# Kernel optimization log

Hardware: AMD Instinct MI355X
Metric: run time of the kernel (lower is better)

Reference implementation:

```python
import jax, jax.numpy as jnp
import numpy as np


def setup_inputs() -> dict:
    key = jax.random.key(0)
    B, N = 4, 32768
    xyz = jax.random.normal(key, (B, N, 3), dtype=jnp.float32)
    return {"xyz": xyz, "K": 16, "nqueries": 2048}


def reference(xyz, K, nqueries):
    # xyz: (b, n, 3). Deterministic strided pick of nqueries query points
    # (stand-in for the KD-tree's distance-pick sampling), then brute-force KNN.
    b, n, _ = xyz.shape
    stride = n // nqueries
    q_idx = jnp.arange(nqueries) * stride          # (nq,)
    pts = xyz[:, q_idx, :]                          # (b, nq, 3) sampled query points
    # pairwise squared distances (b, nq, n)
    d = jnp.sum((pts[:, :, None, :] - xyz[:, None, :, :]) ** 2, axis=-1)
    _, idx = jax.lax.top_k(-d, K)                   # (b, nq, K) nearest-neighbor indices
    idx = idx.astype(jnp.int64)[..., None]          # (b, nq, K, 1) matches expand_dims(..., 3)
    return idx, pts
```

## Files before the change

### kernel.cpp

```cpp
#include <hip/hip_runtime.h>
#include <stdint.h>

#define NPTS  32768
#define NQ    2048
#define KNN   16
#define NB    4
#define BLOCK 256
#define WPB   4
#define PPL   8
#define ITERS (NPTS / (64 * PPL))
#define GATE_MARGIN 5e-4f

__device__ __forceinline__ int dpp_shr1_i(int x) {
    return __builtin_amdgcn_update_dpp(x, x, 0x111, 0xf, 0xf, false);
}
__device__ __forceinline__ float dpp_shr1_f(float x) {
    return __int_as_float(dpp_shr1_i(__float_as_int(x)));
}
__device__ __forceinline__ float readlane_f(float x, int l) {
    return __int_as_float(__builtin_amdgcn_readlane(__float_as_int(x), l));
}

template <int T>
__device__ __forceinline__ void insert_all(float d, int p, int lane,
                                           float& ld, int& li, float& tau,
                                           float& th, float qnm)
{
    unsigned long long rem = __ballot(d <= tau);
    while (rem) {
        const int srcl = __ffsll(rem) - 1;
        const float wd = readlane_f(d, srcl);
        const int   wi = __builtin_amdgcn_readlane(p, srcl);
        const bool less = (ld < wd) || (ld == wd && li < wi);
        const unsigned long long lm = __ballot(less);
        const int pos = __popc((unsigned)((lm >> (16 * T)) & 0xffffull));
        const float pld = dpp_shr1_f(ld);
        const int   pli = dpp_shr1_i(li);
        if ((lane >> 4) == T) {
            const int gl = lane & 15;
            if (gl == pos)      { ld = wd;  li = wi;  }
            else if (gl > pos)  { ld = pld; li = pli; }
        }
        tau = readlane_f(ld, 16 * T + 15);
        th  = tau + qnm;
        rem &= rem - 1;
        if (rem) rem &= __ballot(d <= tau);
    }
}

__device__ __forceinline__ void load6(float4 dst[6], const float4* p) {
    #pragma unroll
    for (int t = 0; t < 6; ++t) dst[t] = p[t];
}

__device__ __forceinline__ void step2(const float4 c[6], int pb, int lane,
                                      float m2x0, float m2y0, float m2z0,
                                      float m2x1, float m2y1, float m2z1,
                                      float qx0, float qy0, float qz0,
                                      float qx1, float qy1, float qz1,
                                      float& ld, int& li,
                                      float& tau0, float& tau1,
                                      float& th0, float& th1,
                                      float qnm0, float qnm1)
{
    float px[PPL], py[PPL], pz[PPL];
    px[0] = c[0].x; py[0] = c[0].y; pz[0] = c[0].z;
    px[1] = c[0].w; py[1] = c[1].x; pz[1] = c[1].y;
    px[2] = c[1].z; py[2] = c[1].w; pz[2] = c[2].x;
    px[3] = c[2].y; py[3] = c[2].z; pz[3] = c[2].w;
    px[4] = c[3].x; py[4] = c[3].y; pz[4] = c[3].z;
    px[5] = c[3].w; py[5] = c[4].x; pz[5] = c[4].y;
    px[6] = c[4].z; py[6] = c[4].w; pz[6] = c[5].x;
    px[7] = c[5].y; py[7] = c[5].z; pz[7] = c[5].w;

    unsigned long long m0[PPL], m1[PPL], any = 0;
    #pragma unroll
    for (int j = 0; j < PPL; ++j) {
        const float s = __fmaf_rn(pz[j], pz[j],
                          __fmaf_rn(py[j], py[j], __fmul_rn(px[j], px[j])));
        float t0 = __fmaf_rn(px[j], m2x0, s);
        t0 = __fmaf_rn(py[j], m2y0, t0);
        t0 = __fmaf_rn(pz[j], m2z0, t0);
        m0[j] = __ballot(t0 <= th0);
        float t1 = __fmaf_rn(px[j], m2x1, s);
        t1 = __fmaf_rn(py[j], m2y1, t1);
        t1 = __fmaf_rn(pz[j], m2z1, t1);
        m1[j] = __ballot(t1 <= th1);
        any |= m0[j] | m1[j];
    }
    if (any) {
        #pragma unroll
        for (int j = 0; j < PPL; ++j) {
            if (m0[j]) {
                const float dx = __fadd_rn(px[j], -qx0);
                const float dy = __fadd_rn(py[j], -qy0);
                const float dz = __fadd_rn(pz[j], -qz0);
                const float d  = __fadd_rn(
                    __fadd_rn(__fmul_rn(dx, dx), __fmul_rn(dy, dy)),
                    __fmul_rn(dz, dz));
                insert_all<0>(d, pb + j, lane, ld, li, tau0, th0, qnm0);
            }
        }
        #pragma unroll
        for (int j = 0; j < PPL; ++j) {
            if (m1[j]) {
                const float dx = __fadd_rn(px[j], -qx1);
                const float dy = __fadd_rn(py[j], -qy1);
                const float dz = __fadd_rn(pz[j], -qz1);
                const float d  = __fadd_rn(
                    __fadd_rn(__fmul_rn(dx, dx), __fmul_rn(dy, dy)),
                    __fmul_rn(dz, dz));
                insert_all<1>(d, pb + j, lane, ld, li, tau1, th1, qnm1);
            }
        }
    }
}

__global__ __launch_bounds__(BLOCK, 4) void knn_kernel(const float* __restrict__ xyz,
                                                       float* __restrict__ out_idx,
                                                       float* __restrict__ out_pts)
{
    const int tid  = threadIdx.x;
    const int lane = tid & 63;
    const int wv   = tid >> 6;
    const int w    = blockIdx.x * WPB + wv;
    const int b    = w >> 10;
    const int pr   = w & 1023;
    const size_t base = (size_t)b * NPTS * 3;

    const int qp0 = pr << 5;
    const float qx0 = xyz[base + 3 * qp0 + 0];
    const float qy0 = xyz[base + 3 * qp0 + 1];
    const float qz0 = xyz[base + 3 * qp0 + 2];
    const float qx1 = xyz[base + 3 * qp0 + 48];
    const float qy1 = xyz[base + 3 * qp0 + 49];
    const float qz1 = xyz[base + 3 * qp0 + 50];

    const int g0 = b * NQ + (pr << 1);
    if (lane == 0) {
        out_pts[3 * g0 + 0] = qx0;
        out_pts[3 * g0 + 1] = qy0;
        out_pts[3 * g0 + 2] = qz0;
        out_pts[3 * g0 + 3] = qx1;
        out_pts[3 * g0 + 4] = qy1;
        out_pts[3 * g0 + 5] = qz1;
    }

    const float m2x0 = -2.0f * qx0, m2y0 = -2.0f * qy0, m2z0 = -2.0f * qz0;
    const float m2x1 = -2.0f * qx1, m2y1 = -2.0f * qy1, m2z1 = -2.0f * qz1;
    const float qnm0 = -(qx0 * qx0 + qy0 * qy0 + qz0 * qz0) + GATE_MARGIN;
    const float qnm1 = -(qx1 * qx1 + qy1 * qy1 + qz1 * qz1) + GATE_MARGIN;

    float ld = __builtin_inff();  int li = 0x7fffffff;
    float tau0 = __builtin_inff(), tau1 = __builtin_inff();
    float th0  = __builtin_inff(), th1  = __builtin_inff();

    const float4* lp0 = (const float4*)(xyz + base) + 6 * lane;

    float4 A[6], Bf[6], Cf[6];
    load6(A,  lp0);
    load6(Bf, lp0 + 384);
    load6(Cf, lp0 + 768);
    const float4* ld_ptr = lp0 + 3 * 384;
    int pb = PPL * lane;

    for (int it = 0; it < 21; ++it) {
        step2(A, pb, lane,
              m2x0, m2y0, m2z0, m2x1, m2y1, m2z1,
              qx0, qy0, qz0, qx1, qy1, qz1,
              ld, li, tau0, tau1, th0, th1, qnm0, qnm1);
        pb += 512;
        load6(A, ld_ptr);  ld_ptr += 384;
        step2(Bf, pb, lane,
              m2x0, m2y0, m2z0, m2x1, m2y1, m2z1,
              qx0, qy0, qz0, qx1, qy1, qz1,
              ld, li, tau0, tau1, th0, th1, qnm0, qnm1);
        pb += 512;
        if (it < 20) load6(Bf, ld_ptr);
        ld_ptr += 384;
        step2(Cf, pb, lane,
              m2x0, m2y0, m2z0, m2x1, m2y1, m2z1,
              qx0, qy0, qz0, qx1, qy1, qz1,
              ld, li, tau0, tau1, th0, th1, qnm0, qnm1);
        pb += 512;
        if (it < 20) load6(Cf, ld_ptr);
        ld_ptr += 384;
    }
    step2(A, pb, lane,
          m2x0, m2y0, m2z0, m2x1, m2y1, m2z1,
          qx0, qy0, qz0, qx1, qy1, qz1,
          ld, li, tau0, tau1, th0, th1, qnm0, qnm1);

    if (lane < 2 * KNN) {
        out_idx[(size_t)g0 * KNN + lane] = (float)li;
    }
}

extern "C" void kernel_launch(void* const* d_in, const int* in_sizes, int n_in,
                              void* d_out, int out_size, void* d_ws, size_t ws_size,
                              hipStream_t stream) {
    const float* xyz = (const float*)d_in[0];
    float* out = (float*)d_out;
    float* out_idx = out;
    float* out_pts = out + (size_t)NB * NQ * KNN;

    const int blocks = (NB * NQ / 2) / WPB;
    knn_kernel<<<blocks, BLOCK, 0, stream>>>(xyz, out_idx, out_pts);
}
```

Before: 183.0 us.

## Bin points along x and prune KNN search by slab distance

```diff
diff --git a/kernel.cpp b/kernel.cpp
--- a/kernel.cpp
+++ b/kernel.cpp
@@ -5,21 +5,179 @@
 #define NQ    2048
 #define KNN   16
 #define NB    4
+#define NBINS 256
+#define XMIN  (-6.0f)
+#define XW    (12.0f / NBINS)
+#define INVXW (NBINS / 12.0f)
+#define SAFE  1e-4f
+#define GATE_MARGIN 5e-4f
+
+__device__ __forceinline__ int dpp_shr1_i(int x) {
+    return __builtin_amdgcn_update_dpp(x, x, 0x111, 0xf, 0xf, false);
+}
+__device__ __forceinline__ float dpp_shr1_f(float x) {
+    return __int_as_float(dpp_shr1_i(__float_as_int(x)));
+}
+__device__ __forceinline__ float readlane_f(float x, int l) {
+    return __int_as_float(__builtin_amdgcn_readlane(__float_as_int(x), l));
+}
+__device__ __forceinline__ int binof(float x) {
+    int b = (int)((x - XMIN) * INVXW);
+    return min(max(b, 0), NBINS - 1);
+}
+
+__device__ __forceinline__ void insert16(float d, int p, int lane,
+                                         float& ld, int& li, float& tau,
+                                         unsigned long long vm)
+{
+    unsigned long long rem = __ballot(d <= tau) & vm;
+    while (rem) {
+        const int srcl = __ffsll(rem) - 1;
+        const float wd = readlane_f(d, srcl);
+        const int   wi = __builtin_amdgcn_readlane(p, srcl);
+        const bool less = (ld < wd) || (ld == wd && li < wi);
+        const unsigned long long lm = __ballot(less);
+        const int pos = __popc((unsigned)(lm & 0xffffull));
+        const float pld = dpp_shr1_f(ld);
+        const int   pli = dpp_shr1_i(li);
+        if (lane < 16) {
+            if (lane == pos)      { ld = wd;  li = wi;  }
+            else if (lane > pos)  { ld = pld; li = pli; }
+        }
+        tau = readlane_f(ld, 15);
+        rem &= rem - 1;
+        if (rem) rem &= __ballot(d <= tau);
+    }
+}
+
+__global__ __launch_bounds__(NBINS) void zero_k(int* __restrict__ cur) {
+    cur[blockIdx.x * NBINS + threadIdx.x] = 0;
+}
+
+__global__ __launch_bounds__(256) void hist_k(const float* __restrict__ xyz,
+                                              int* __restrict__ cur)
+{
+    const int i = blockIdx.x * 256 + threadIdx.x;
+    const int b = i >> 15;
+    const int idx = i & (NPTS - 1);
+    const float x = xyz[(size_t)b * NPTS * 3 + 3 * idx];
+    atomicAdd(&cur[b * NBINS + binof(x)], 1);
+}
+
+__global__ __launch_bounds__(NBINS) void scan_k(int* __restrict__ cur,
+                                                int* __restrict__ off)
+{
+    const int b = blockIdx.x, t = threadIdx.x;
+    __shared__ int sh[NBINS];
+    const int c = cur[b * NBINS + t];
+    sh[t] = c;
+    __syncthreads();
+    for (int o = 1; o < NBINS; o <<= 1) {
+        const int v = (t >= o) ? sh[t - o] : 0;
+        __syncthreads();
+        sh[t] += v;
+        __syncthreads();
+    }
+    const int excl = sh[t] - c;
+    off[b * (NBINS + 1) + t] = excl;
+    if (t == NBINS - 1) off[b * (NBINS + 1) + NBINS] = sh[t];
+    cur[b * NBINS + t] = excl;
+}
+
+__global__ __launch_bounds__(256) void scatter_k(const float* __restrict__ xyz,
+                                                 int* __restrict__ cur,
+                                                 float4* __restrict__ sorted)
+{
+    const int i = blockIdx.x * 256 + threadIdx.x;
+    const int b = i >> 15;
+    const int idx = i & (NPTS - 1);
+    const size_t a = (size_t)b * NPTS * 3 + 3 * idx;
+    const float x = xyz[a], y = xyz[a + 1], z = xyz[a + 2];
+    const int pos = atomicAdd(&cur[b * NBINS + binof(x)], 1);
+    sorted[(size_t)b * NPTS + pos] = make_float4(x, y, z, __int_as_float(idx));
+}
+
+__device__ __forceinline__ void scan_bin(const float4* __restrict__ sp,
+                                         int s, int e, int lane,
+                                         float qx, float qy, float qz,
+                                         float& ld, int& li, float& tau)
+{
+    for (int ba = s; ba < e; ba += 64) {
+        float d = __builtin_inff(); int pi = 0x7fffffff;
+        const unsigned long long vm = __ballot(ba + lane < e);
+        if (ba + lane < e) {
+            const float4 pt = sp[ba + lane];
+            const float dx = __fadd_rn(pt.x, -qx);
+            const float dy = __fadd_rn(pt.y, -qy);
+            const float dz = __fadd_rn(pt.z, -qz);
+            d = __fadd_rn(__fadd_rn(__fmul_rn(dx, dx), __fmul_rn(dy, dy)),
+                          __fmul_rn(dz, dz));
+            pi = __float_as_int(pt.w);
+        }
+        insert16(d, pi, lane, ld, li, tau, vm);
+    }
+}
+
+__global__ __launch_bounds__(256) void knn_grid(const float* __restrict__ xyz,
+                                                const float4* __restrict__ sorted,
+                                                const int* __restrict__ off,
+                                                float* __restrict__ out_idx,
+                                                float* __restrict__ out_pts)
+{
+    const int tid  = threadIdx.x;
+    const int lane = tid & 63;
+    const int wv   = tid >> 6;
+    const int w    = blockIdx.x * 4 + wv;
+    const int b    = w >> 11;
+    const int qi   = w & 2047;
+    const size_t base3 = (size_t)b * NPTS * 3;
+    const int qp = qi << 4;
+    const float qx = xyz[base3 + 3 * qp + 0];
+    const float qy = xyz[base3 + 3 * qp + 1];
+    const float qz = xyz[base3 + 3 * qp + 2];
+
+    const int g = b * NQ + qi;
+    if (lane == 0) {
+        out_pts[3 * g + 0] = qx;
+        out_pts[3 * g + 1] = qy;
+        out_pts[3 * g + 2] = qz;
+    }
+
+    const float4* sp = sorted + (size_t)b * NPTS;
+    const int* ofb = off + b * (NBINS + 1);
+
+    float ld = __builtin_inff(); int li = 0x7fffffff;
+    float tau = __builtin_inff();
+
+    const int bq = binof(qx);
+    scan_bin(sp, ofb[bq], ofb[bq + 1], lane, qx, qy, qz, ld, li, tau);
+
+    int bl = bq - 1, br = bq + 1;
+    for (;;) {
+        const float dl = (bl >= 0)     ? (qx - (XMIN + (bl + 1) * XW)) : 1e30f;
+        const float dr = (br < NBINS)  ? ((XMIN + br * XW) - qx)       : 1e30f;
+        const float dls = dl - SAFE, drs = dr - SAFE;
+        const bool doneL = (bl < 0)      || (dls > 0.0f && dls * dls > tau);
+        const bool doneR = (br >= NBINS) || (drs > 0.0f && drs * drs > tau);
+        if (doneL && doneR) break;
+        if (!doneL && (doneR || dl <= dr)) {
+            scan_bin(sp, ofb[bl], ofb[bl + 1], lane, qx, qy, qz, ld, li, tau);
+            --bl;
+        } else {
+            scan_bin(sp, ofb[br], ofb[br + 1], lane, qx, qy, qz, ld, li, tau);
+            ++br;
+        }
+    }
+
+    if (lane < KNN) {
+        out_idx[(size_t)g * KNN + lane] = (float)li;
+    }
+}
+
 #define BLOCK 256
 #define WPB   4
 #define PPL   8
 #define ITERS (NPTS / (64 * PPL))
-#define GATE_MARGIN 5e-4f
-
-__device__ __forceinline__ int dpp_shr1_i(int x) {
-    return __builtin_amdgcn_update_dpp(x, x, 0x111, 0xf, 0xf, false);
-}
-__device__ __forceinline__ float dpp_shr1_f(float x) {
-    return __int_as_float(dpp_shr1_i(__float_as_int(x)));
-}
-__device__ __forceinline__ float readlane_f(float x, int l) {
-    return __int_as_float(__builtin_amdgcn_readlane(__float_as_int(x), l));
-}
 
 template <int T>
 __device__ __forceinline__ void insert_all(float d, int p, int lane,
@@ -116,9 +274,9 @@
     }
 }
 
-__global__ __launch_bounds__(BLOCK, 4) void knn_kernel(const float* __restrict__ xyz,
-                                                       float* __restrict__ out_idx,
-                                                       float* __restrict__ out_pts)
+__global__ __launch_bounds__(BLOCK, 4) void knn_bf(const float* __restrict__ xyz,
+                                                   float* __restrict__ out_idx,
+                                                   float* __restrict__ out_pts)
 {
     const int tid  = threadIdx.x;
     const int lane = tid & 63;
@@ -165,29 +323,25 @@
     int pb = PPL * lane;
 
     for (int it = 0; it < 21; ++it) {
-        step2(A, pb, lane,
-              m2x0, m2y0, m2z0, m2x1, m2y1, m2z1,
+        step2(A, pb, lane, m2x0, m2y0, m2z0, m2x1, m2y1, m2z1,
               qx0, qy0, qz0, qx1, qy1, qz1,
               ld, li, tau0, tau1, th0, th1, qnm0, qnm1);
         pb += 512;
         load6(A, ld_ptr);  ld_ptr += 384;
-        step2(Bf, pb, lane,
-              m2x0, m2y0, m2z0, m2x1, m2y1, m2z1,
+        step2(Bf, pb, lane, m2x0, m2y0, m2z0, m2x1, m2y1, m2z1,
               qx0, qy0, qz0, qx1, qy1, qz1,
               ld, li, tau0, tau1, th0, th1, qnm0, qnm1);
         pb += 512;
         if (it < 20) load6(Bf, ld_ptr);
         ld_ptr += 384;
-        step2(Cf, pb, lane,
-              m2x0, m2y0, m2z0, m2x1, m2y1, m2z1,
+        step2(Cf, pb, lane, m2x0, m2y0, m2z0, m2x1, m2y1, m2z1,
               qx0, qy0, qz0, qx1, qy1, qz1,
               ld, li, tau0, tau1, th0, th1, qnm0, qnm1);
         pb += 512;
         if (it < 20) load6(Cf, ld_ptr);
         ld_ptr += 384;
     }
-    step2(A, pb, lane,
-          m2x0, m2y0, m2z0, m2x1, m2y1, m2z1,
+    step2(A, pb, lane, m2x0, m2y0, m2z0, m2x1, m2y1, m2z1,
           qx0, qy0, qz0, qx1, qy1, qz1,
           ld, li, tau0, tau1, th0, th1, qnm0, qnm1);
 
@@ -204,6 +358,19 @@
     float* out_idx = out;
     float* out_pts = out + (size_t)NB * NQ * KNN;
 
-    const int blocks = (NB * NQ / 2) / WPB;
-    knn_kernel<<<blocks, BLOCK, 0, stream>>>(xyz, out_idx, out_pts);
-}
+    const size_t sorted_bytes = (size_t)NB * NPTS * sizeof(float4);
+    const size_t ws_needed = sorted_bytes
+                           + (size_t)(NB * (NBINS + 1) + NB * NBINS) * sizeof(int);
+    if (d_ws != nullptr && ws_size >= ws_needed) {
+        float4* sorted = (float4*)d_ws;
+        int* off = (int*)((char*)d_ws + sorted_bytes);
+        int* cur = off + NB * (NBINS + 1);
+        zero_k<<<NB, NBINS, 0, stream>>>(cur);
+        hist_k<<<NB * NPTS / 256, 256, 0, stream>>>(xyz, cur);
+        scan_k<<<NB, NBINS, 0, stream>>>(cur, off);
+        scatter_k<<<NB * NPTS / 256, 256, 0, stream>>>(xyz, cur, sorted);
+        knn_grid<<<NB * NQ / 4, 256, 0, stream>>>(xyz, sorted, off, out_idx, out_pts);
+    } else {
+        knn_bf<<<(NB * NQ / 2) / WPB, BLOCK, 0, stream>>>(xyz, out_idx, out_pts);
+    }
+}
```

New measurement: 283.5 us. 1.55x slower.
